# Performance work log

Hardware: AMD Instinct MI355X
Metric: run time of the kernel (lower is better)

Reference implementation:

```python
import jax, jax.numpy as jnp
import numpy as np
from jax import lax

SEQ, BATCH, INPUT, HIDDEN = 2048, 32, 256, 256


def setup_inputs() -> dict:
    key = jax.random.key(0)
    k1, k2, k3 = jax.random.split(key, 3)
    scale = 1.0 / np.sqrt(HIDDEN)
    return {
        "input": jax.random.normal(k1, (SEQ, BATCH, INPUT), dtype=jnp.float32),
        "W_ih": jax.random.normal(k2, (3 * HIDDEN, INPUT), dtype=jnp.float32) * scale,
        "W_hh": jax.random.normal(k3, (3 * HIDDEN, HIDDEN), dtype=jnp.float32) * scale,
        "b_ih": jnp.zeros((3 * HIDDEN,), dtype=jnp.float32),
        "b_hh": jnp.zeros((3 * HIDDEN,), dtype=jnp.float32),
    }


def reference(input, W_ih, W_hh, b_ih, b_hh):
    """Single-layer unidirectional CustomGRU forward.

    Faithful to the torch module, including its quirk: the n-gate gets the
    W_hh_n @ h contribution twice (once un-gated via `gates`, once gated by r).
    Returns (output [S,B,H], h_n [1,B,H]).
    """
    H = W_hh.shape[0] // 3
    W_hn = W_hh[2 * H:]  # [H, H]
    # Precompute input projections for all timesteps (same math, batched GEMM).
    x_proj = jnp.einsum('sbi,gi->sbg', input, W_ih) + b_ih + b_hh  # [S,B,3H]

    def step(h, xp):
        gates = xp + h @ W_hh.T  # [B, 3H]
        r, z, n = jnp.split(gates, 3, axis=1)
        r = jax.nn.sigmoid(r)
        z = jax.nn.sigmoid(z)
        n = jnp.tanh(n + r * (h @ W_hn.T))
        h_new = (1.0 - z) * n + z * h
        return h_new, h_new

    h0 = jnp.zeros((input.shape[1], H), dtype=input.dtype)
    h_last, output = lax.scan(step, h0, x_proj)
    return output, h_last[None, :, :]
```

## Files before the change

kernel.cpp:

```cpp
#include <hip/hip_runtime.h>
#include <stdint.h>
#include <stddef.h>

#define S_LEN 2048
#define BATCH 32
#define NIN   256
#define NH    256
#define NG    768
#define GRUB  32
#define XPB   2048

typedef _Float16 half2_t __attribute__((ext_vector_type(2)));
typedef int      int8v   __attribute__((ext_vector_type(8)));
typedef int      int4v   __attribute__((ext_vector_type(4)));

#if __has_builtin(__builtin_amdgcn_exp2f)
#define EXP2F(x) __builtin_amdgcn_exp2f(x)
#else
#define EXP2F(x) exp2f(x)
#endif

static __device__ __forceinline__ float fdot2(half2_t a, half2_t b, float c) {
  return __builtin_amdgcn_fdot2(a, b, c, false);
}
static __device__ __forceinline__ half2_t pack2(float lo, float hi) {
  half2_t r; r[0] = (_Float16)lo; r[1] = (_Float16)hi; return r;
}
static __device__ __forceinline__ float sigmoid_fast(float x) {
  float e = EXP2F(-1.44269504088896340736f * x);
  return 1.0f / (1.0f + e);
}
static __device__ __forceinline__ float tanh_fast(float x) {
  float e = EXP2F(2.88539008177792681472f * x);
  return 1.0f - 2.0f / (1.0f + e);
}
static __device__ __forceinline__ float dpp_xor1(float v) {
  return __builtin_bit_cast(float,
    __builtin_amdgcn_mov_dpp(__builtin_bit_cast(int, v), 0xB1, 0xF, 0xF, true));
}
static __device__ __forceinline__ float dpp_xor2(float v) {
  return __builtin_bit_cast(float,
    __builtin_amdgcn_mov_dpp(__builtin_bit_cast(int, v), 0x4E, 0xF, 0xF, true));
}

static __device__ __forceinline__ int flags_all36(const int* p) {
  int4v a0, a1, a2, a3, a4, a5, a6, a7, a8;
  asm volatile("global_load_dwordx4 %0, %9, off sc0 sc1\n"
               "global_load_dwordx4 %1, %9, off offset:16 sc0 sc1\n"
               "global_load_dwordx4 %2, %9, off offset:32 sc0 sc1\n"
               "global_load_dwordx4 %3, %9, off offset:48 sc0 sc1\n"
               "global_load_dwordx4 %4, %9, off offset:64 sc0 sc1\n"
               "global_load_dwordx4 %5, %9, off offset:80 sc0 sc1\n"
               "global_load_dwordx4 %6, %9, off offset:96 sc0 sc1\n"
               "global_load_dwordx4 %7, %9, off offset:112 sc0 sc1\n"
               "global_load_dwordx4 %8, %9, off offset:128 sc0 sc1\n"
               "s_waitcnt vmcnt(0)"
               : "=v"(a0), "=v"(a1), "=v"(a2), "=v"(a3), "=v"(a4),
                 "=v"(a5), "=v"(a6), "=v"(a7), "=v"(a8)
               : "v"(p)
               : "memory");
  int all = a0.x & a0.y & a0.z & a0.w;
  all &= a1.x & a1.y & a1.z & a1.w;
  all &= a2.x & a2.y & a2.z & a2.w;
  all &= a3.x & a3.y & a3.z & a3.w;
  all &= a4.x & a4.y & a4.z & a4.w;
  all &= a5.x & a5.y & a5.z & a5.w;
  all &= a6.x & a6.y & a6.z & a6.w;
  all &= a7.x & a7.y & a7.z & a7.w;
  all &= a8.x & a8.y & a8.z & a8.w;
  return all;
}
#define FLAGWAIT36(BASEP) do {                                                \
    while (!flags_all36(BASEP)) __builtin_amdgcn_s_sleep(16);                 \
  } while (0)

#define BH(x)    __builtin_bit_cast(half2_t, (x))
#define BW(W, e) __builtin_bit_cast(half2_t, (int)((W)[e]))
#define P2I(a, b) __builtin_bit_cast(int, pack2((a), (b)))

#define DOT6(q, U0, U1, U2, U3, U4, U5, o) do {                               \
    a0 = fdot2(BW(U0,(o)+0), BH(q.x), a0); a1 = fdot2(BW(U1,(o)+0), BH(q.x), a1);\
    a2 = fdot2(BW(U2,(o)+0), BH(q.x), a2); a3 = fdot2(BW(U3,(o)+0), BH(q.x), a3);\
    a4 = fdot2(BW(U4,(o)+0), BH(q.x), a4); a5 = fdot2(BW(U5,(o)+0), BH(q.x), a5);\
    a0 = fdot2(BW(U0,(o)+1), BH(q.y), a0); a1 = fdot2(BW(U1,(o)+1), BH(q.y), a1);\
    a2 = fdot2(BW(U2,(o)+1), BH(q.y), a2); a3 = fdot2(BW(U3,(o)+1), BH(q.y), a3);\
    a4 = fdot2(BW(U4,(o)+1), BH(q.y), a4); a5 = fdot2(BW(U5,(o)+1), BH(q.y), a5);\
    a0 = fdot2(BW(U0,(o)+2), BH(q.z), a0); a1 = fdot2(BW(U1,(o)+2), BH(q.z), a1);\
    a2 = fdot2(BW(U2,(o)+2), BH(q.z), a2); a3 = fdot2(BW(U3,(o)+2), BH(q.z), a3);\
    a4 = fdot2(BW(U4,(o)+2), BH(q.z), a4); a5 = fdot2(BW(U5,(o)+2), BH(q.z), a5);\
    a0 = fdot2(BW(U0,(o)+3), BH(q.w), a0); a1 = fdot2(BW(U1,(o)+3), BH(q.w), a1);\
    a2 = fdot2(BW(U2,(o)+3), BH(q.w), a2); a3 = fdot2(BW(U3,(o)+3), BH(q.w), a3);\
    a4 = fdot2(BW(U4,(o)+3), BH(q.w), a4); a5 = fdot2(BW(U5,(o)+3), BH(q.w), a5);\
  } while (0)

#define LDW8(W, o) do {                                                       \
    int4 t0 = wsrc[(o)], t1 = wsrc[(o) + 1];                                  \
    W = (int8v){t0.x, t0.y, t0.z, t0.w, t1.x, t1.y, t1.z, t1.w};              \
  } while (0)

#define LOADPIN_W(SRC)                                                        \
  int8v W00, W01, W02, W03, W10, W11, W12, W13, W20, W21, W22, W23,           \
        W30, W31, W32, W33, W40, W41, W42, W43, W50, W51, W52, W53;           \
  {                                                                           \
    const int4* wsrc = (const int4*)(SRC);                                    \
    LDW8(W00, 0);  LDW8(W01, 2);  LDW8(W02, 4);  LDW8(W03, 6);                \
    LDW8(W10, 8);  LDW8(W11, 10); LDW8(W12, 12); LDW8(W13, 14);               \
    LDW8(W20, 16); LDW8(W21, 18); LDW8(W22, 20); LDW8(W23, 22);               \
    LDW8(W30, 24); LDW8(W31, 26); LDW8(W32, 28); LDW8(W33, 30);               \
    LDW8(W40, 32); LDW8(W41, 34); LDW8(W42, 36); LDW8(W43, 38);               \
    LDW8(W50, 40); LDW8(W51, 42); LDW8(W52, 44); LDW8(W53, 46);               \
  }                                                                           \
  asm volatile("" : "+v"(W00), "+v"(W01), "+v"(W02), "+v"(W03),               \
                    "+v"(W10), "+v"(W11), "+v"(W12), "+v"(W13),               \
                    "+v"(W20), "+v"(W21), "+v"(W22), "+v"(W23),               \
                    "+v"(W30), "+v"(W31), "+v"(W32), "+v"(W33),               \
                    "+v"(W40), "+v"(W41), "+v"(W42), "+v"(W43),               \
                    "+v"(W50), "+v"(W51), "+v"(W52), "+v"(W53));

#define QREDUCE(MVR, MVZ, MVN) do {                                           \
    float b0 = a0 + dpp_xor1(a0), b1 = a1 + dpp_xor1(a1);                     \
    float b2 = a2 + dpp_xor1(a2), b3 = a3 + dpp_xor1(a3);                     \
    float b4 = a4 + dpp_xor1(a4), b5 = a5 + dpp_xor1(a5);                     \
    float xr_ = jj ? b1 : b0, xz_ = jj ? b3 : b2, xn_ = jj ? b5 : b4;         \
    MVR = xr_ + dpp_xor2(xr_);                                                \
    MVZ = xz_ + dpp_xor2(xz_);                                                \
    MVN = xn_ + dpp_xor2(xn_);                                                \
  } while (0)

__global__ __launch_bounds__(256) void prep_w_kernel(const float* __restrict__ W_ih,
                                                     const float* __restrict__ W_hh,
                                                     const float* __restrict__ b_ih,
                                                     const float* __restrict__ b_hh,
                                                     half2_t* __restrict__ whh3,
                                                     half2_t* __restrict__ wih3,
                                                     float* __restrict__ bias,
                                                     int* __restrict__ flags) {
  int idx = blockIdx.x * 256 + threadIdx.x;
  if (idx < 128 * NG) {
    int tid = idx / 192;
    int r   = idx - tid * 192;
    int d   = r >> 5, kk = r & 31;
    int gate = d >> 1, jj = d & 1;
    int c  = tid & 3, j1 = tid >> 2;
    int row = gate * NH + 2 * j1 + jj;
    int col = 64 * c + 2 * kk;
    whh3[idx] = pack2(W_hh[(size_t)row * NH + col], W_hh[(size_t)row * NH + col + 1]);
  } else if (idx < 2 * 128 * NG) {
    int i2  = idx - 128 * NG;
    int tid = i2 / 192;
    int r   = i2 - tid * 192;
    int d   = r >> 5, kk = r & 31;
    int gate = d >> 1, jj = d & 1;
    int c  = tid & 3, j1 = tid >> 2;
    int row = gate * NH + 2 * j1 + jj;
    int col = 64 * c + 2 * kk;
    wih3[i2] = pack2(W_ih[(size_t)row * NIN + col], W_ih[(size_t)row * NIN + col + 1]);
  } else if (idx < 2 * 128 * NG + NG) {
    int g = idx - 2 * 128 * NG;
    bias[g] = b_ih[g] + b_hh[g];
  } else if (idx < 2 * 128 * NG + NG + XPB + 16) {
    int k = idx - (2 * 128 * NG + NG);
    flags[k] = (k < XPB) ? 0 : 1;
  }
}

__global__
__attribute__((amdgpu_flat_work_group_size(512, 512), amdgpu_waves_per_eu(2, 2)))
void fused_kernel(const float* __restrict__ inf,
                  const half2_t* __restrict__ wih3,
                  const float* __restrict__ bias,
                  float* __restrict__ xp,
                  const half2_t* __restrict__ whh3,
                  float* __restrict__ out,
                  int* __restrict__ flags) {
  const int tid = threadIdx.x;
  const int c   = tid & 3;
  const int j1  = tid >> 2;
  const int jj  = c & 1;
  const int jmine = 2 * j1 + jj;

  if (blockIdx.x >= GRUB) {
    const int xb = (int)blockIdx.x - GRUB;
    LOADPIN_W(wih3 + (size_t)tid * 192);
    const float bgr = bias[jmine], bgz = bias[NH + jmine], bgn = bias[2 * NH + jmine];
    const float4* fr = (const float4*)(inf + (size_t)xb * 32 * NIN + c * 64);
    float* xo = xp + (size_t)xb * 32 * NG + jmine;
    for (int rr = 0; rr < 32; ++rr) {
      float a0 = 0.f, a1 = 0.f, a2 = 0.f, a3 = 0.f, a4 = 0.f, a5 = 0.f;
      float4 g0, g1; int4 q;
#define XB(IDX, U0, U1, U2, U3, U4, U5, OFF)                                  \
      g0 = fr[2 * (IDX)]; g1 = fr[2 * (IDX) + 1];                             \
      q.x = P2I(g0.x, g0.y); q.y = P2I(g0.z, g0.w);                           \
      q.z = P2I(g1.x, g1.y); q.w = P2I(g1.z, g1.w);                           \
      DOT6(q, U0, U1, U2, U3, U4, U5, OFF);
      XB(0, W00, W10, W20, W30, W40, W50, 0)
      XB(1, W00, W10, W20, W30, W40, W50, 4)
      XB(2, W01, W11, W21, W31, W41, W51, 0)
      XB(3, W01, W11, W21, W31, W41, W51, 4)
      XB(4, W02, W12, W22, W32, W42, W52, 0)
      XB(5, W02, W12, W22, W32, W42, W52, 4)
      XB(6, W03, W13, W23, W33, W43, W53, 0)
      XB(7, W03, W13, W23, W33, W43, W53, 4)
#undef XB
      float mvr, mvz, mvn;
      QREDUCE(mvr, mvz, mvn);
      if (c < 2) {
        float vr = mvr + bgr, vz = mvz + bgz, vn = mvn + bgn;
        asm volatile("global_store_dword %0, %1, off sc0 sc1\n"
                     "global_store_dword %0, %2, off offset:1024 sc0 sc1\n"
                     "global_store_dword %0, %3, off offset:2048 sc0 sc1"
                     :: "v"(xo), "v"(vr), "v"(vz), "v"(vn) : "memory");
      }
      fr += 64;
      xo += NG;
    }
    __syncthreads();
    if (tid == 0) {
      int one = 1;
      asm volatile("global_store_dword %0, %1, off sc0 sc1"
                   :: "v"(&flags[xb]), "v"(one) : "memory");
    }
    return;
  }

  const int b = blockIdx.x;
  LOADPIN_W(whh3 + (size_t)tid * 192);

  __shared__ __attribute__((aligned(16))) char smh[1152];
  if (tid < 288) ((int*)smh)[tid] = 0;

  FLAGWAIT36(flags);

  const float* xq = xp + (size_t)b * NG + jmine;
  float xr_c = xq[0], xz_c = xq[NH], xn_c = xq[2 * NH];
  xq += (size_t)BATCH * NG;
  float* op = out + (size_t)b * NH + jmine;

  const int wofs = 144 * (jmine >> 6) + 2 * (jmine & 63);

  float h = 0.f;
  __syncthreads();

#define GSTEP(RB, WB) do {                                                    \
    float xr_n = xq[0], xz_n = xq[NH], xn_n = xq[2 * NH];                     \
    const int4* hb4 = (const int4*)(smh + (RB) + c * 144);                    \
    float a0 = 0.f, a1 = 0.f, a2 = 0.f, a3 = 0.f, a4 = 0.f, a5 = 0.f;        \
    int4 qa0 = hb4[0], qa1 = hb4[1];                                          \
    int4 qb0 = hb4[2], qb1 = hb4[3];                                          \
    DOT6(qa0, W00, W10, W20, W30, W40, W50, 0);                               \
    DOT6(qa1, W00, W10, W20, W30, W40, W50, 4);                               \
    qa0 = hb4[4]; qa1 = hb4[5];                                               \
    DOT6(qb0, W01, W11, W21, W31, W41, W51, 0);                               \
    DOT6(qb1, W01, W11, W21, W31, W41, W51, 4);                               \
    qb0 = hb4[6]; qb1 = hb4[7];                                               \
    DOT6(qa0, W02, W12, W22, W32, W42, W52, 0);                               \
    DOT6(qa1, W02, W12, W22, W32, W42, W52, 4);                               \
    DOT6(qb0, W03, W13, W23, W33, W43, W53, 0);                               \
    DOT6(qb1, W03, W13, W23, W33, W43, W53, 4);                               \
    float mvr, mvz, mvn;                                                      \
    QREDUCE(mvr, mvz, mvn);                                                   \
    float r = sigmoid_fast(xr_c + mvr);                                       \
    float z = sigmoid_fast(xz_c + mvz);                                       \
    float n = tanh_fast(xn_c + mvn + r * mvn);              \
    h = z * (h - n) + n;                                                      \
    if (c < 2) {                                                              \
      op[0] = h;                                                              \
      *(_Float16*)(smh + (WB) + wofs) = (_Float16)h;                          \
    }                                                                         \
    asm volatile("s_waitcnt lgkmcnt(0)\n\ts_barrier" ::: "memory");           \
    xr_c = xr_n; xz_c = xz_n; xn_c = xn_n;                                    \
    xq += (size_t)BATCH * NG;                                                 \
    op += (size_t)BATCH * NH;                                                 \
  } while (0)

  for (int t0 = 0; t0 < S_LEN; t0 += 8) {
    if (t0 && (t0 & 31) == 0) FLAGWAIT36(flags + t0);
    for (int u = 0; u < 4; ++u) {
      GSTEP(0, 576);
      GSTEP(576, 0);
    }
  }
#undef GSTEP

  if (c < 2) out[(size_t)S_LEN * BATCH * NH + (size_t)b * NH + jmine] = h;
}

extern "C" void kernel_launch(void* const* d_in, const int* in_sizes, int n_in,
                              void* d_out, int out_size, void* d_ws, size_t ws_size,
                              hipStream_t stream) {
  const float* input = (const float*)d_in[0];
  const float* W_ih  = (const float*)d_in[1];
  const float* W_hh  = (const float*)d_in[2];
  const float* b_ih  = (const float*)d_in[3];
  const float* b_hh  = (const float*)d_in[4];
  float* out = (float*)d_out;

  const size_t SB = (size_t)S_LEN * BATCH;
  const size_t xp_b = SB * NG * 4;
  const size_t w_b  = (size_t)128 * NG * 4;

  char* p = (char*)d_ws;
  float*    xp    = (float*)p;                p += xp_b;
  half2_t*  whh3  = (half2_t*)p;              p += w_b;
  half2_t*  wih3  = (half2_t*)p;              p += w_b;
  float*    bias  = (float*)p;                p += (size_t)NG * 4;
  uintptr_t fp_ = (((uintptr_t)p) + 127) & ~(uintptr_t)127;
  int*      flags = (int*)fp_;

  const int prep_items = 2 * 128 * NG + NG + XPB + 16;
  prep_w_kernel<<<(prep_items + 255) / 256, 256, 0, stream>>>(W_ih, W_hh, b_ih, b_hh,
                                                              whh3, wih3, bias, flags);
  fused_kernel<<<GRUB + XPB, 512, 0, stream>>>(input, wih3, bias, xp, whh3, out, flags);
  (void)out_size; (void)n_in; (void)in_sizes; (void)ws_size;
}
```

Measured before the change: 2.345 ms.

## Move one third of pinned weights from registers into LDS

Moves the last two gate-row groups of each thread's weight slice out of pinned VGPRs into a 128 KB shared-memory buffer. The projection and recurrent inner loops now read those weights from LDS, with loads interleaved with the fdot2 chains. This lowers register pressure, possibly removing spills, but adds LDS traffic on the serial recurrent critical path and allocates a large LDS buffer per block.

```diff
diff --git a/kernel.cpp b/kernel.cpp
--- a/kernel.cpp
+++ b/kernel.cpp
@@ -78,19 +78,19 @@
 #define BW(W, e) __builtin_bit_cast(half2_t, (int)((W)[e]))
 #define P2I(a, b) __builtin_bit_cast(int, pack2((a), (b)))
 
-#define DOT6(q, U0, U1, U2, U3, U4, U5, o) do {                               \
+#define DOT6H(q, U0, U1, U2, U3, o, L4, L5) do {                              \
     a0 = fdot2(BW(U0,(o)+0), BH(q.x), a0); a1 = fdot2(BW(U1,(o)+0), BH(q.x), a1);\
     a2 = fdot2(BW(U2,(o)+0), BH(q.x), a2); a3 = fdot2(BW(U3,(o)+0), BH(q.x), a3);\
-    a4 = fdot2(BW(U4,(o)+0), BH(q.x), a4); a5 = fdot2(BW(U5,(o)+0), BH(q.x), a5);\
+    a4 = fdot2(BW(L4,0), BH(q.x), a4);     a5 = fdot2(BW(L5,0), BH(q.x), a5); \
     a0 = fdot2(BW(U0,(o)+1), BH(q.y), a0); a1 = fdot2(BW(U1,(o)+1), BH(q.y), a1);\
     a2 = fdot2(BW(U2,(o)+1), BH(q.y), a2); a3 = fdot2(BW(U3,(o)+1), BH(q.y), a3);\
-    a4 = fdot2(BW(U4,(o)+1), BH(q.y), a4); a5 = fdot2(BW(U5,(o)+1), BH(q.y), a5);\
+    a4 = fdot2(BW(L4,1), BH(q.y), a4);     a5 = fdot2(BW(L5,1), BH(q.y), a5); \
     a0 = fdot2(BW(U0,(o)+2), BH(q.z), a0); a1 = fdot2(BW(U1,(o)+2), BH(q.z), a1);\
     a2 = fdot2(BW(U2,(o)+2), BH(q.z), a2); a3 = fdot2(BW(U3,(o)+2), BH(q.z), a3);\
-    a4 = fdot2(BW(U4,(o)+2), BH(q.z), a4); a5 = fdot2(BW(U5,(o)+2), BH(q.z), a5);\
+    a4 = fdot2(BW(L4,2), BH(q.z), a4);     a5 = fdot2(BW(L5,2), BH(q.z), a5); \
     a0 = fdot2(BW(U0,(o)+3), BH(q.w), a0); a1 = fdot2(BW(U1,(o)+3), BH(q.w), a1);\
     a2 = fdot2(BW(U2,(o)+3), BH(q.w), a2); a3 = fdot2(BW(U3,(o)+3), BH(q.w), a3);\
-    a4 = fdot2(BW(U4,(o)+3), BH(q.w), a4); a5 = fdot2(BW(U5,(o)+3), BH(q.w), a5);\
+    a4 = fdot2(BW(L4,3), BH(q.w), a4);     a5 = fdot2(BW(L5,3), BH(q.w), a5); \
   } while (0)
 
 #define LDW8(W, o) do {                                                       \
@@ -98,24 +98,28 @@
     W = (int8v){t0.x, t0.y, t0.z, t0.w, t1.x, t1.y, t1.z, t1.w};              \
   } while (0)
 
-#define LOADPIN_W(SRC)                                                        \
-  int8v W00, W01, W02, W03, W10, W11, W12, W13, W20, W21, W22, W23,           \
-        W30, W31, W32, W33, W40, W41, W42, W43, W50, W51, W52, W53;           \
+#define LOADPIN_W128(SRC)                                                     \
+  int8v W00, W01, W02, W03, W10, W11, W12, W13,                               \
+        W20, W21, W22, W23, W30, W31, W32, W33;                               \
   {                                                                           \
     const int4* wsrc = (const int4*)(SRC);                                    \
     LDW8(W00, 0);  LDW8(W01, 2);  LDW8(W02, 4);  LDW8(W03, 6);                \
     LDW8(W10, 8);  LDW8(W11, 10); LDW8(W12, 12); LDW8(W13, 14);               \
     LDW8(W20, 16); LDW8(W21, 18); LDW8(W22, 20); LDW8(W23, 22);               \
     LDW8(W30, 24); LDW8(W31, 26); LDW8(W32, 28); LDW8(W33, 30);               \
-    LDW8(W40, 32); LDW8(W41, 34); LDW8(W42, 36); LDW8(W43, 38);               \
-    LDW8(W50, 40); LDW8(W51, 42); LDW8(W52, 44); LDW8(W53, 46);               \
   }                                                                           \
   asm volatile("" : "+v"(W00), "+v"(W01), "+v"(W02), "+v"(W03),               \
                     "+v"(W10), "+v"(W11), "+v"(W12), "+v"(W13),               \
                     "+v"(W20), "+v"(W21), "+v"(W22), "+v"(W23),               \
-                    "+v"(W30), "+v"(W31), "+v"(W32), "+v"(W33),               \
-                    "+v"(W40), "+v"(W41), "+v"(W42), "+v"(W43),               \
-                    "+v"(W50), "+v"(W51), "+v"(W52), "+v"(W53));
+                    "+v"(W30), "+v"(W31), "+v"(W32), "+v"(W33));
+
+#define STAGE_WLDS(SRC)                                                       \
+  {                                                                           \
+    const int4v* ws4 = (const int4v*)(SRC);                                   \
+    int4v* wl = ((int4v*)wsmem) + tid;                                        \
+    _Pragma("unroll")                                                         \
+    for (int s = 0; s < 16; ++s) wl[s * 512] = ws4[32 + s];                   \
+  }
 
 #define QREDUCE(MVR, MVZ, MVN) do {                                           \
     float b0 = a0 + dpp_xor1(a0), b1 = a1 + dpp_xor1(a1);                     \
@@ -179,29 +183,34 @@
   const int jj  = c & 1;
   const int jmine = 2 * j1 + jj;
 
+  __shared__ __attribute__((aligned(16))) char wsmem[131072];
+  const int4v* wlt = ((const int4v*)wsmem) + tid;
+
   if (blockIdx.x >= GRUB) {
     const int xb = (int)blockIdx.x - GRUB;
-    LOADPIN_W(wih3 + (size_t)tid * 192);
+    LOADPIN_W128(wih3 + (size_t)tid * 192);
+    STAGE_WLDS(wih3 + (size_t)tid * 192);
     const float bgr = bias[jmine], bgz = bias[NH + jmine], bgn = bias[2 * NH + jmine];
     const float4* fr = (const float4*)(inf + (size_t)xb * 32 * NIN + c * 64);
     float* xo = xp + (size_t)xb * 32 * NG + jmine;
     for (int rr = 0; rr < 32; ++rr) {
       float a0 = 0.f, a1 = 0.f, a2 = 0.f, a3 = 0.f, a4 = 0.f, a5 = 0.f;
-      float4 g0, g1; int4 q;
-#define XB(IDX, U0, U1, U2, U3, U4, U5, OFF)                                  \
+      float4 g0, g1; int4 q; int4v l4, l5;
+#define XC(IDX, U0, U1, U2, U3, OFF)                                          \
       g0 = fr[2 * (IDX)]; g1 = fr[2 * (IDX) + 1];                             \
+      l4 = wlt[(IDX) * 512]; l5 = wlt[((IDX) + 8) * 512];                     \
       q.x = P2I(g0.x, g0.y); q.y = P2I(g0.z, g0.w);                           \
       q.z = P2I(g1.x, g1.y); q.w = P2I(g1.z, g1.w);                           \
-      DOT6(q, U0, U1, U2, U3, U4, U5, OFF);
-      XB(0, W00, W10, W20, W30, W40, W50, 0)
-      XB(1, W00, W10, W20, W30, W40, W50, 4)
-      XB(2, W01, W11, W21, W31, W41, W51, 0)
-      XB(3, W01, W11, W21, W31, W41, W51, 4)
-      XB(4, W02, W12, W22, W32, W42, W52, 0)
-      XB(5, W02, W12, W22, W32, W42, W52, 4)
-      XB(6, W03, W13, W23, W33, W43, W53, 0)
-      XB(7, W03, W13, W23, W33, W43, W53, 4)
-#undef XB
+      DOT6H(q, U0, U1, U2, U3, OFF, l4, l5);
+      XC(0, W00, W10, W20, W30, 0)
+      XC(1, W00, W10, W20, W30, 4)
+      XC(2, W01, W11, W21, W31, 0)
+      XC(3, W01, W11, W21, W31, 4)
+      XC(4, W02, W12, W22, W32, 0)
+      XC(5, W02, W12, W22, W32, 4)
+      XC(6, W03, W13, W23, W33, 0)
+      XC(7, W03, W13, W23, W33, 4)
+#undef XC
       float mvr, mvz, mvn;
       QREDUCE(mvr, mvz, mvn);
       if (c < 2) {
@@ -224,7 +233,8 @@
   }
 
   const int b = blockIdx.x;
-  LOADPIN_W(whh3 + (size_t)tid * 192);
+  LOADPIN_W128(whh3 + (size_t)tid * 192);
+  STAGE_WLDS(whh3 + (size_t)tid * 192);
 
   __shared__ __attribute__((aligned(16))) char smh[1152];
   if (tid < 288) ((int*)smh)[tid] = 0;
@@ -245,18 +255,25 @@
     float xr_n = xq[0], xz_n = xq[NH], xn_n = xq[2 * NH];                     \
     const int4* hb4 = (const int4*)(smh + (RB) + c * 144);                    \
     float a0 = 0.f, a1 = 0.f, a2 = 0.f, a3 = 0.f, a4 = 0.f, a5 = 0.f;        \
-    int4 qa0 = hb4[0], qa1 = hb4[1];                                          \
-    int4 qb0 = hb4[2], qb1 = hb4[3];                                          \
-    DOT6(qa0, W00, W10, W20, W30, W40, W50, 0);                               \
-    DOT6(qa1, W00, W10, W20, W30, W40, W50, 4);                               \
+    int4 qa0 = hb4[0], qa1 = hb4[1], qb0 = hb4[2], qb1 = hb4[3];              \
+    int4v lA = wlt[0 * 512], lB = wlt[8 * 512];                               \
+    int4v lC = wlt[1 * 512], lD = wlt[9 * 512];                               \
+    DOT6H(qa0, W00, W10, W20, W30, 0, lA, lB);                                \
+    lA = wlt[2 * 512]; lB = wlt[10 * 512];                                    \
+    DOT6H(qa1, W00, W10, W20, W30, 4, lC, lD);                                \
     qa0 = hb4[4]; qa1 = hb4[5];                                               \
-    DOT6(qb0, W01, W11, W21, W31, W41, W51, 0);                               \
-    DOT6(qb1, W01, W11, W21, W31, W41, W51, 4);                               \
+    lC = wlt[3 * 512]; lD = wlt[11 * 512];                                    \
+    DOT6H(qb0, W01, W11, W21, W31, 0, lA, lB);                                \
+    lA = wlt[4 * 512]; lB = wlt[12 * 512];                                    \
+    DOT6H(qb1, W01, W11, W21, W31, 4, lC, lD);                                \
     qb0 = hb4[6]; qb1 = hb4[7];                                               \
-    DOT6(qa0, W02, W12, W22, W32, W42, W52, 0);                               \
-    DOT6(qa1, W02, W12, W22, W32, W42, W52, 4);                               \
-    DOT6(qb0, W03, W13, W23, W33, W43, W53, 0);                               \
-    DOT6(qb1, W03, W13, W23, W33, W43, W53, 4);                               \
+    lC = wlt[5 * 512]; lD = wlt[13 * 512];                                    \
+    DOT6H(qa0, W02, W12, W22, W32, 0, lA, lB);                                \
+    lA = wlt[6 * 512]; lB = wlt[14 * 512];                                    \
+    DOT6H(qa1, W02, W12, W22, W32, 4, lC, lD);                                \
+    lC = wlt[7 * 512]; lD = wlt[15 * 512];                                    \
+    DOT6H(qb0, W03, W13, W23, W33, 0, lA, lB);                                \
+    DOT6H(qb1, W03, W13, W23, W33, 4, lC, lD);                                \
     float mvr, mvz, mvn;                                                      \
     QREDUCE(mvr, mvz, mvn);                                                   \
     float r = sigmoid_fast(xr_c + mvr);                                       \
```

New measurement: 2.523 ms. 7.6% more time.
